# Optimization experiments

Measured on AMD Instinct MI355X. Metric: run time of the kernel, lower is better.

The kernel has to match this reference:

```python
import jax, jax.numpy as jnp
import numpy as np

EMB_DIM = 1024
HEAD_SIZE = 64
B, T = 4, 4096


def setup_inputs() -> dict:
    key = jax.random.key(0)
    kx, kq, kk, kv = jax.random.split(key, 4)
    scale = 1.0 / np.sqrt(EMB_DIM)
    x = jax.random.normal(kx, (B, T, EMB_DIM), dtype=jnp.float32)
    # weights stored as [emb_dim, head_size] so projection is x @ W
    Wq = jax.random.normal(kq, (EMB_DIM, HEAD_SIZE), dtype=jnp.float32) * scale
    Wk = jax.random.normal(kk, (EMB_DIM, HEAD_SIZE), dtype=jnp.float32) * scale
    Wv = jax.random.normal(kv, (EMB_DIM, HEAD_SIZE), dtype=jnp.float32) * scale
    return {"x": x, "Wq": Wq, "Wk": Wk, "Wv": Wv}


def reference(x, Wq, Wk, Wv):
    # Single causal self-attention head. NOTE: original scales by emb_dim**-0.5
    # (d = x.shape[-1]), not head_size**-0.5 — we reproduce that faithfully.
    _, t, d = x.shape
    q = jnp.einsum('bte,eh->bth', x, Wq)
    k = jnp.einsum('bte,eh->bth', x, Wk)
    v = jnp.einsum('bte,eh->bth', x, Wv)
    wei = jnp.einsum('bth,bsh->bts', q, k) * (d ** -0.5)  # [B, T, T]
    causal = jnp.tril(jnp.ones((t, t), dtype=bool))
    wei = jnp.where(causal, wei, -jnp.inf)
    attn = jax.nn.softmax(wei, axis=-1)
    out = jnp.einsum('bts,bsh->bth', attn, v)  # [B, T, head_size]
    return out
```

## Files before the change

### kernel.cpp

```cpp
#include <hip/hip_runtime.h>
#include <hip/hip_bf16.h>

#define EMB   1024
#define HS    64
#define BATCH 4
#define SEQ   4096
#define MTOT  (BATCH*SEQ)

typedef float  f32x4 __attribute__((ext_vector_type(4)));
typedef short  s16x8 __attribute__((ext_vector_type(8)));
typedef __bf16 bf16x8 __attribute__((ext_vector_type(8)));

__device__ __forceinline__ unsigned short f2bf(float f) {
    unsigned int u = __float_as_uint(f);
    u = (u + 0x7fffu + ((u >> 16) & 1u)) >> 16;
    return (unsigned short)u;
}
__device__ __forceinline__ unsigned int pkbf(float lo, float hi) {
#if __has_builtin(__builtin_amdgcn_cvt_pk_bf16_f32)
    return __builtin_bit_cast(unsigned int,
        __builtin_amdgcn_cvt_pk_bf16_f32(lo, hi));
#else
    return (unsigned int)f2bf(lo) | ((unsigned int)f2bf(hi) << 16);
#endif
}
__device__ __forceinline__ s16x8 cvt8(float4 a, float4 b) {
    union { unsigned int u[4]; s16x8 v; } r;
    r.u[0] = pkbf(a.x, a.y); r.u[1] = pkbf(a.z, a.w);
    r.u[2] = pkbf(b.x, b.y); r.u[3] = pkbf(b.z, b.w);
    return r.v;
}
__device__ __forceinline__ f32x4 mfma16(s16x8 a, s16x8 b, f32x4 c) {
    return __builtin_amdgcn_mfma_f32_16x16x32_bf16(
        __builtin_bit_cast(bf16x8, a), __builtin_bit_cast(bf16x8, b), c, 0, 0, 0);
}
__device__ __forceinline__ void ld_lds16(const void* g, unsigned short* l) {
    __builtin_amdgcn_global_load_lds(
        (const __attribute__((address_space(1))) unsigned int*)g,
        (__attribute__((address_space(3))) unsigned int*)l, 16, 0, 0);
}

__global__ __launch_bounds__(256) void pack_w(const float* __restrict__ Wq,
                                              const float* __restrict__ Wk,
                                              const float* __restrict__ Wv,
                                              unsigned short* __restrict__ wp) {
    int idx = blockIdx.x * 256 + threadIdx.x;
    int l = idx & 63;
    int s = (idx >> 6) & 31;
    int t = idx >> 11;
    const float* W = (t < 4) ? Wq : (t < 8) ? Wk : Wv;
    float scale = (t < 4) ? 0.03125f : 1.0f;
    int n  = ((t & 3) * 16) + (l & 15);
    int k0 = s * 32 + ((l >> 4) * 8);
    s16x8 v;
#pragma unroll
    for (int j = 0; j < 8; j++)
        v[j] = (short)f2bf(W[(size_t)(k0 + j) * HS + n] * scale);
    *(s16x8*)(wp + (size_t)idx * 8) = v;
}

__global__ __launch_bounds__(256) void proj(const float* __restrict__ x,
                                            const unsigned short* __restrict__ wp,
                                            unsigned short* __restrict__ qws,
                                            unsigned short* __restrict__ kws,
                                            unsigned short* __restrict__ vtws) {
    __shared__ unsigned short xb[2][2][2048];
    __shared__ unsigned short wb2[2][12288];
    __shared__ unsigned short vt[32][72];
    int l = threadIdx.x & 63, w = threadIdx.x >> 6;
    int lane15 = l & 15, quad = l >> 4;
    int rh = w & 1, ts = w >> 1;
    int row0 = blockIdx.x * 32;

    auto stage = [&](int buf, int sg2) {
        int d = w * 64 + l;
        int row = d >> 3, cs = d & 7;
        int sc = cs ^ (row & 7);
#pragma unroll
        for (int sp = 0; sp < 2; sp++)
            ld_lds16(x + (size_t)(row0 + row) * EMB + sg2 * 64 + sp * 32 + sc * 4,
                     &xb[buf][sp][w * 512]);
#pragma unroll
        for (int j = 0; j < 6; j++) {
            int f = w + 4 * j;
            int sp = f / 12, t = f % 12;
            ld_lds16(wp + ((size_t)(t * 32 + sg2 * 2 + sp) * 64 + l) * 8,
                     &wb2[buf][f * 512]);
        }
    };

    int xrow = rh * 16 + lane15;
    int rsw = xrow & 7;
    f32x4 acc[6] = {};

    stage(0, 0);
    int buf = 0;
    for (int sg2 = 0; sg2 < 16; sg2++) {
        __syncthreads();
        if (sg2 < 15) stage(buf ^ 1, sg2 + 1);

#pragma unroll
        for (int sp = 0; sp < 2; sp++) {
            float4 lo = *(const float4*)&xb[buf][sp][(xrow * 8 + ((2 * quad)     ^ rsw)) * 8];
            float4 hi = *(const float4*)&xb[buf][sp][(xrow * 8 + ((2 * quad + 1) ^ rsw)) * 8];
            s16x8 af = cvt8(lo, hi);
#pragma unroll
            for (int j = 0; j < 6; j++) {
                int t = ts + 2 * j;
                s16x8 bfr = *(const s16x8*)&wb2[buf][(sp * 12 + t) * 512 + l * 8];
                acc[j] = mfma16(af, bfr, acc[j]);
            }
        }
        buf ^= 1;
    }

#pragma unroll
    for (int r = 0; r < 4; r++) {
        int row = row0 + rh * 16 + quad * 4 + r;
#pragma unroll
        for (int j = 0; j < 2; j++) {
            int tq = ts + 2 * j;
            qws[(size_t)row * HS + tq * 16 + lane15] = f2bf(acc[j][r]);
            kws[(size_t)row * HS + tq * 16 + lane15] = f2bf(acc[j + 2][r]);
            vt[rh * 16 + quad * 4 + r][tq * 16 + lane15] = f2bf(acc[j + 4][r]);
        }
    }
    __syncthreads();
    if (threadIdx.x < 128) {
        int h = threadIdx.x & 63, half = threadIdx.x >> 6;
        int b = row0 >> 12, tp0 = row0 & (SEQ - 1);
        unsigned short tmp[16];
#pragma unroll
        for (int j = 0; j < 16; j++) tmp[j] = vt[half * 16 + j][h];
        unsigned short* dst = vtws + ((size_t)b * HS + h) * SEQ + tp0 + half * 16;
        *(s16x8*)dst       = *(s16x8*)tmp;
        *(s16x8*)(dst + 8) = *(s16x8*)(tmp + 8);
    }
}

__global__ __launch_bounds__(256) void attn_part(const unsigned short* __restrict__ qws,
                                                 const unsigned short* __restrict__ kws,
                                                 const unsigned short* __restrict__ vtws,
                                                 float* __restrict__ op,
                                                 float* __restrict__ lp) {
    __shared__ unsigned short ldsK[2][2][4096];
    __shared__ unsigned short ldsV[2][2][4096];
    __shared__ unsigned short plds[4][16][72];

    int l = threadIdx.x & 63;
    int w = threadIdx.x >> 6;
    int lane15 = l & 15, quad = l >> 4;

    int W = blockIdx.x;
    int b = W / 288;
    int g = W - b * 288;
    int n = 1;
    while (g >= 4 * n * (n + 1)) n++;
    int off = g - 4 * n * (n - 1);
    int oQ  = (unsigned)off / (unsigned)n;
    int Q   = 8 * (n - 1) + oQ;
    int c   = off - oQ * n;
    int lenT = Q + 1;
    int t0 = c * 8;
    int t1 = min(t0 + 8, lenT);
    int q0 = Q * 64 + w * 16;
    int diag = lenT - 1;

    auto stagePair = [&](int buf, int p0) {
#pragma unroll
        for (int ti = 0; ti < 2; ti++) {
            int c0 = min(p0 + ti, SEQ / 64 - 1) * 64;
#pragma unroll
            for (int j = 0; j < 2; j++) {
                int s = w + j * 4;
                int t = s >> 1, h = s & 1;
                ld_lds16(kws + ((size_t)b * SEQ + c0 + t * 16 + lane15) * HS
                             + h * 32 + quad * 8,
                         &ldsK[buf][ti][s * 512]);
                ld_lds16(vtws + ((size_t)b * HS + t * 16 + lane15) * SEQ
                              + c0 + h * 32 + quad * 8,
                         &ldsV[buf][ti][s * 512]);
            }
        }
    };

    const unsigned short* qbase =
        qws + ((size_t)b * SEQ + q0 + lane15) * HS + quad * 8;
    s16x8 qf0 = *(const s16x8*)(qbase);
    s16x8 qf1 = *(const s16x8*)(qbase + 32);

    f32x4 o[4] = {};
    float lsum[4] = {0.f, 0.f, 0.f, 0.f};

    auto body = [&](int kt, const unsigned short* Kb, const unsigned short* Vb) {
        f32x4 sacc[4] = {};
#pragma unroll
        for (int t = 0; t < 4; t++) {
            s16x8 kf0 = *(const s16x8*)(Kb + (2 * t) * 512 + l * 8);
            s16x8 kf1 = *(const s16x8*)(Kb + (2 * t + 1) * 512 + l * 8);
            sacc[t] = mfma16(qf0, kf0, sacc[t]);
            sacc[t] = mfma16(qf1, kf1, sacc[t]);
        }
        if (kt == diag) {
            int c0 = kt * 64;
#pragma unroll
            for (int t = 0; t < 4; t++)
#pragma unroll
                for (int r = 0; r < 4; r++) {
                    int qrow = q0 + quad * 4 + r;
                    int kcol = c0 + t * 16 + lane15;
                    if (kcol > qrow) sacc[t][r] = -1e30f;
                }
        }
#pragma unroll
        for (int t = 0; t < 4; t++)
#pragma unroll
            for (int r = 0; r < 4; r++) {
                float p = __expf(sacc[t][r]);
                lsum[r] += p;
                plds[w][quad * 4 + r][t * 16 + lane15] = f2bf(p);
            }
        __builtin_amdgcn_s_waitcnt(0xC07F);
#pragma unroll
        for (int c2 = 0; c2 < 2; c2++) {
            s16x8 pf = *(const s16x8*)(&plds[w][lane15][c2 * 32 + quad * 8]);
#pragma unroll
            for (int t = 0; t < 4; t++) {
                s16x8 vf = *(const s16x8*)(Vb + (2 * t + c2) * 512 + l * 8);
                o[t] = mfma16(pf, vf, o[t]);
            }
        }
    };

    stagePair(0, t0);
    int buf = 0;
    for (int kt = t0; kt < t1; kt += 2) {
        __syncthreads();
        if (kt + 2 < t1) stagePair(buf ^ 1, kt + 2);
        body(kt, ldsK[buf][0], ldsV[buf][0]);
        if (kt + 1 < t1) body(kt + 1, ldsK[buf][1], ldsV[buf][1]);
        buf ^= 1;
    }

#pragma unroll
    for (int r = 0; r < 4; r++) {
#pragma unroll
        for (int d = 1; d < 16; d <<= 1)
            lsum[r] += __shfl_xor(lsum[r], d, 64);
    }

    size_t slot = (size_t)b * 288 + g;
    float* ob = op + slot * 4096;
#pragma unroll
    for (int t = 0; t < 4; t++)
#pragma unroll
        for (int r = 0; r < 4; r++)
            ob[(w * 16 + quad * 4 + r) * 64 + t * 16 + lane15] = o[t][r];
    if (lane15 == 0) {
#pragma unroll
        for (int r = 0; r < 4; r++)
            lp[slot * 64 + w * 16 + quad * 4 + r] = lsum[r];
    }
}

__global__ __launch_bounds__(256) void attn_combine(const float* __restrict__ op,
                                                    const float* __restrict__ lp,
                                                    float* __restrict__ out) {
    int e = blockIdx.x * 256 + threadIdx.x;
    int c4 = (e & 15) * 4;
    int row = e >> 4;
    int b   = row >> 12;
    int tr  = row & (SEQ - 1);
    int Q   = tr >> 6;
    int r64 = tr & 63;
    int n   = (Q >> 3) + 1;
    int g0  = 4 * n * (n - 1) + (Q - 8 * (n - 1)) * n;
    f32x4 os = {0.f, 0.f, 0.f, 0.f};
    float ls = 0.f;
    for (int c = 0; c < n; c++) {
        size_t slot = (size_t)b * 288 + g0 + c;
        os += *(const f32x4*)(op + slot * 4096 + r64 * 64 + c4);
        ls += lp[slot * 64 + r64];
    }
    f32x4 r = os / ls;
    *(f32x4*)(out + (size_t)row * HS + c4) = r;
}

extern "C" void kernel_launch(void* const* d_in, const int* in_sizes, int n_in,
                              void* d_out, int out_size, void* d_ws, size_t ws_size,
                              hipStream_t stream) {
    const float* x  = (const float*)d_in[0];
    const float* Wq = (const float*)d_in[1];
    const float* Wk = (const float*)d_in[2];
    const float* Wv = (const float*)d_in[3];
    float* out = (float*)d_out;

    unsigned short* ws   = (unsigned short*)d_ws;
    unsigned short* wp   = ws;
    unsigned short* qws  = ws + 262144;
    unsigned short* kws  = ws + 1310720;
    unsigned short* vtws = ws + 2359296;
    float* op = (float*)(ws + 3407872);
    float* lp = op + 4718592;

    hipLaunchKernelGGL(pack_w,      dim3(96),   dim3(256), 0, stream, Wq, Wk, Wv, wp);
    hipLaunchKernelGGL(proj,        dim3(512),  dim3(256), 0, stream, x, wp, qws, kws, vtws);
    hipLaunchKernelGGL(attn_part,   dim3(1152), dim3(256), 0, stream, qws, kws, vtws, op, lp);
    hipLaunchKernelGGL(attn_combine,dim3(1024), dim3(256), 0, stream, op, lp, out);
}
```

Baseline: 156.6 us.

## Warp-specialize attention: dedicated producer wave feeds 4-deep K/V ring via LDS flags

The attention kernel gains a fifth wavefront that only issues async global-to-LDS loads of K and V tiles into a 4-slot ring buffer. The four compute waves consume each tile after spinning on per-slot ready counters and signal completion through done counters. Block-wide __syncthreads barriers are gone, so the compute waves no longer stall in lockstep with staging. In exchange the kernel uses more LDS and adds spin-wait polling with s_sleep, which could lower occupancy or add latency. Correctness depends on the vmcnt-based ordering of the async LDS loads.

```diff
diff --git a/kernel.cpp b/kernel.cpp
--- a/kernel.cpp
+++ b/kernel.cpp
@@ -6,6 +6,8 @@
 #define BATCH 4
 #define SEQ   4096
 #define MTOT  (BATCH*SEQ)
+
+#define WAIT_LGKM0() asm volatile("s_waitcnt lgkmcnt(0)" ::: "memory")
 
 typedef float  f32x4 __attribute__((ext_vector_type(4)));
 typedef short  s16x8 __attribute__((ext_vector_type(8)));
@@ -38,6 +40,10 @@
     __builtin_amdgcn_global_load_lds(
         (const __attribute__((address_space(1))) unsigned int*)g,
         (__attribute__((address_space(3))) unsigned int*)l, 16, 0, 0);
+}
+__device__ __forceinline__ void wg_wait_ge(unsigned int* p, unsigned int tok) {
+    while (__hip_atomic_load(p, __ATOMIC_ACQUIRE, __HIP_MEMORY_SCOPE_WORKGROUP) < tok)
+        __builtin_amdgcn_s_sleep(1);
 }
 
 __global__ __launch_bounds__(256) void pack_w(const float* __restrict__ Wq,
@@ -98,7 +104,6 @@
     for (int sg2 = 0; sg2 < 16; sg2++) {
         __syncthreads();
         if (sg2 < 15) stage(buf ^ 1, sg2 + 1);
-
 #pragma unroll
         for (int sp = 0; sp < 2; sp++) {
             float4 lo = *(const float4*)&xb[buf][sp][(xrow * 8 + ((2 * quad)     ^ rsw)) * 8];
@@ -138,14 +143,15 @@
     }
 }
 
-__global__ __launch_bounds__(256) void attn_part(const unsigned short* __restrict__ qws,
+__global__ __launch_bounds__(320) void attn_part(const unsigned short* __restrict__ qws,
                                                  const unsigned short* __restrict__ kws,
                                                  const unsigned short* __restrict__ vtws,
                                                  float* __restrict__ op,
                                                  float* __restrict__ lp) {
-    __shared__ unsigned short ldsK[2][2][4096];
-    __shared__ unsigned short ldsV[2][2][4096];
+    __shared__ unsigned short ldsKV[4][2][4096];
     __shared__ unsigned short plds[4][16][72];
+    __shared__ unsigned int ready[4];
+    __shared__ unsigned int done[4];
 
     int l = threadIdx.x & 63;
     int w = threadIdx.x >> 6;
@@ -163,103 +169,122 @@
     int lenT = Q + 1;
     int t0 = c * 8;
     int t1 = min(t0 + 8, lenT);
-    int q0 = Q * 64 + w * 16;
+    int steps = t1 - t0;
     int diag = lenT - 1;
 
-    auto stagePair = [&](int buf, int p0) {
-#pragma unroll
-        for (int ti = 0; ti < 2; ti++) {
-            int c0 = min(p0 + ti, SEQ / 64 - 1) * 64;
-#pragma unroll
-            for (int j = 0; j < 2; j++) {
-                int s = w + j * 4;
-                int t = s >> 1, h = s & 1;
+    if (threadIdx.x < 4) { ready[threadIdx.x] = 0; done[threadIdx.x] = 0; }
+    __syncthreads();
+
+    if (w == 4) {
+        auto issue_tile = [&](int buf, int kt) {
+            int c0 = kt * 64;
+#pragma unroll
+            for (int s2 = 0; s2 < 8; s2++) {
+                int t = s2 >> 1, h = s2 & 1;
                 ld_lds16(kws + ((size_t)b * SEQ + c0 + t * 16 + lane15) * HS
                              + h * 32 + quad * 8,
-                         &ldsK[buf][ti][s * 512]);
+                         &ldsKV[buf][0][s2 * 512]);
+            }
+#pragma unroll
+            for (int s2 = 0; s2 < 8; s2++) {
+                int t = s2 >> 1, h = s2 & 1;
                 ld_lds16(vtws + ((size_t)b * HS + t * 16 + lane15) * SEQ
                               + c0 + h * 32 + quad * 8,
-                         &ldsV[buf][ti][s * 512]);
-            }
-        }
-    };
-
-    const unsigned short* qbase =
-        qws + ((size_t)b * SEQ + q0 + lane15) * HS + quad * 8;
-    s16x8 qf0 = *(const s16x8*)(qbase);
-    s16x8 qf1 = *(const s16x8*)(qbase + 32);
-
-    f32x4 o[4] = {};
-    float lsum[4] = {0.f, 0.f, 0.f, 0.f};
-
-    auto body = [&](int kt, const unsigned short* Kb, const unsigned short* Vb) {
-        f32x4 sacc[4] = {};
-#pragma unroll
-        for (int t = 0; t < 4; t++) {
-            s16x8 kf0 = *(const s16x8*)(Kb + (2 * t) * 512 + l * 8);
-            s16x8 kf1 = *(const s16x8*)(Kb + (2 * t + 1) * 512 + l * 8);
-            sacc[t] = mfma16(qf0, kf0, sacc[t]);
-            sacc[t] = mfma16(qf1, kf1, sacc[t]);
-        }
-        if (kt == diag) {
-            int c0 = kt * 64;
+                         &ldsKV[buf][1][s2 * 512]);
+            }
+        };
+        for (int s = 0; s < steps; s++) {
+            int buf = s & 3;
+            if (s >= 4)
+                wg_wait_ge(&done[buf], 4u * (unsigned)(s >> 2));
+            issue_tile(buf, t0 + s);
+            if (s >= 1) {
+                asm volatile("s_waitcnt vmcnt(16)" ::: "memory");
+                __hip_atomic_store(&ready[(s - 1) & 3], (unsigned)s,
+                                   __ATOMIC_RELEASE, __HIP_MEMORY_SCOPE_WORKGROUP);
+            }
+        }
+        asm volatile("s_waitcnt vmcnt(0)" ::: "memory");
+        __hip_atomic_store(&ready[(steps - 1) & 3], (unsigned)steps,
+                           __ATOMIC_RELEASE, __HIP_MEMORY_SCOPE_WORKGROUP);
+    } else {
+        int q0 = Q * 64 + w * 16;
+        const unsigned short* qbase =
+            qws + ((size_t)b * SEQ + q0 + lane15) * HS + quad * 8;
+        s16x8 qf0 = *(const s16x8*)(qbase);
+        s16x8 qf1 = *(const s16x8*)(qbase + 32);
+
+        f32x4 o[4] = {};
+        float lsum[4] = {0.f, 0.f, 0.f, 0.f};
+
+        for (int s = 0; s < steps; s++) {
+            int buf = s & 3;
+            int kt = t0 + s;
+            wg_wait_ge(&ready[buf], (unsigned)(s + 1));
+            const unsigned short* Kb = ldsKV[buf][0];
+            const unsigned short* Vb = ldsKV[buf][1];
+
+            f32x4 sacc[4] = {};
+#pragma unroll
+            for (int t = 0; t < 4; t++) {
+                s16x8 kf0 = *(const s16x8*)(Kb + (2 * t) * 512 + l * 8);
+                s16x8 kf1 = *(const s16x8*)(Kb + (2 * t + 1) * 512 + l * 8);
+                sacc[t] = mfma16(qf0, kf0, sacc[t]);
+                sacc[t] = mfma16(qf1, kf1, sacc[t]);
+            }
+            if (kt == diag) {
+                int c0 = kt * 64;
+#pragma unroll
+                for (int t = 0; t < 4; t++)
+#pragma unroll
+                    for (int r = 0; r < 4; r++) {
+                        int qrow = q0 + quad * 4 + r;
+                        int kcol = c0 + t * 16 + lane15;
+                        if (kcol > qrow) sacc[t][r] = -1e30f;
+                    }
+            }
 #pragma unroll
             for (int t = 0; t < 4; t++)
 #pragma unroll
                 for (int r = 0; r < 4; r++) {
-                    int qrow = q0 + quad * 4 + r;
-                    int kcol = c0 + t * 16 + lane15;
-                    if (kcol > qrow) sacc[t][r] = -1e30f;
+                    float p = __expf(sacc[t][r]);
+                    lsum[r] += p;
+                    plds[w][quad * 4 + r][t * 16 + lane15] = f2bf(p);
                 }
-        }
+            WAIT_LGKM0();
+#pragma unroll
+            for (int c2 = 0; c2 < 2; c2++) {
+                s16x8 pf = *(const s16x8*)(&plds[w][lane15][c2 * 32 + quad * 8]);
+#pragma unroll
+                for (int t = 0; t < 4; t++) {
+                    s16x8 vf = *(const s16x8*)(Vb + (2 * t + c2) * 512 + l * 8);
+                    o[t] = mfma16(pf, vf, o[t]);
+                }
+            }
+            WAIT_LGKM0();
+            __hip_atomic_fetch_add(&done[buf], 1u,
+                                   __ATOMIC_RELEASE, __HIP_MEMORY_SCOPE_WORKGROUP);
+        }
+
+#pragma unroll
+        for (int r = 0; r < 4; r++) {
+#pragma unroll
+            for (int d = 1; d < 16; d <<= 1)
+                lsum[r] += __shfl_xor(lsum[r], d, 64);
+        }
+
+        size_t slot = (size_t)b * 288 + g;
+        float* ob = op + slot * 4096;
 #pragma unroll
         for (int t = 0; t < 4; t++)
 #pragma unroll
-            for (int r = 0; r < 4; r++) {
-                float p = __expf(sacc[t][r]);
-                lsum[r] += p;
-                plds[w][quad * 4 + r][t * 16 + lane15] = f2bf(p);
-            }
-        __builtin_amdgcn_s_waitcnt(0xC07F);
-#pragma unroll
-        for (int c2 = 0; c2 < 2; c2++) {
-            s16x8 pf = *(const s16x8*)(&plds[w][lane15][c2 * 32 + quad * 8]);
-#pragma unroll
-            for (int t = 0; t < 4; t++) {
-                s16x8 vf = *(const s16x8*)(Vb + (2 * t + c2) * 512 + l * 8);
-                o[t] = mfma16(pf, vf, o[t]);
-            }
-        }
-    };
-
-    stagePair(0, t0);
-    int buf = 0;
-    for (int kt = t0; kt < t1; kt += 2) {
-        __syncthreads();
-        if (kt + 2 < t1) stagePair(buf ^ 1, kt + 2);
-        body(kt, ldsK[buf][0], ldsV[buf][0]);
-        if (kt + 1 < t1) body(kt + 1, ldsK[buf][1], ldsV[buf][1]);
-        buf ^= 1;
-    }
-
-#pragma unroll
-    for (int r = 0; r < 4; r++) {
-#pragma unroll
-        for (int d = 1; d < 16; d <<= 1)
-            lsum[r] += __shfl_xor(lsum[r], d, 64);
-    }
-
-    size_t slot = (size_t)b * 288 + g;
-    float* ob = op + slot * 4096;
-#pragma unroll
-    for (int t = 0; t < 4; t++)
-#pragma unroll
-        for (int r = 0; r < 4; r++)
-            ob[(w * 16 + quad * 4 + r) * 64 + t * 16 + lane15] = o[t][r];
-    if (lane15 == 0) {
-#pragma unroll
-        for (int r = 0; r < 4; r++)
-            lp[slot * 64 + w * 16 + quad * 4 + r] = lsum[r];
+            for (int r = 0; r < 4; r++)
+                ob[(w * 16 + quad * 4 + r) * 64 + t * 16 + lane15] = o[t][r];
+        if (lane15 == 0) {
+#pragma unroll
+            for (int r = 0; r < 4; r++)
+                lp[slot * 64 + w * 16 + quad * 4 + r] = lsum[r];
+        }
     }
 }
 
@@ -305,6 +330,6 @@
 
     hipLaunchKernelGGL(pack_w,      dim3(96),   dim3(256), 0, stream, Wq, Wk, Wv, wp);
     hipLaunchKernelGGL(proj,        dim3(512),  dim3(256), 0, stream, x, wp, qws, kws, vtws);
-    hipLaunchKernelGGL(attn_part,   dim3(1152), dim3(256), 0, stream, qws, kws, vtws, op, lp);
+    hipLaunchKernelGGL(attn_part,   dim3(1152), dim3(320), 0, stream, qws, kws, vtws, op, lp);
     hipLaunchKernelGGL(attn_combine,dim3(1024), dim3(256), 0, stream, op, lp, out);
 }
```

Result: faster. 150.9 us (-3.7%).
